# Optimization experiments

Measured on AMD Instinct MI355X. Metric: run time of the kernel, lower is better.

The kernel has to match this reference:

```python
import jax, jax.numpy as jnp
import numpy as np

N, FIN, F, H = 4096, 128, 64, 8
NEG = -1e10


def setup_inputs() -> dict:
    key = jax.random.key(0)
    ks = jax.random.split(key, 6)
    X = jax.random.normal(ks[0], (N, FIN), dtype=jnp.float32)
    # sparse-ish binary adjacency with self loops, stored dense (as the layer expects)
    A = (jax.random.uniform(ks[1], (N, N)) < 0.05).astype(jnp.int32)
    A = A.at[jnp.arange(N), jnp.arange(N)].set(1)
    W = jax.random.normal(ks[2], (H, FIN, F), dtype=jnp.float32) * (1.0 / np.sqrt(FIN))
    b = jnp.zeros((H, F), dtype=jnp.float32)
    a_self = jax.random.normal(ks[3], (H, F), dtype=jnp.float32) * (1.0 / np.sqrt(F))
    a_neigh = jax.random.normal(ks[4], (H, F), dtype=jnp.float32) * (1.0 / np.sqrt(F))
    return {"X": X, "A": A, "W": W, "b": b, "a_self": a_self, "a_neigh": a_neigh}


def reference(X, A, W, b, a_self, a_neigh):
    # Dropout layers run in inference mode in the original call -> identity.
    feats = jnp.einsum('nf,hfo->hno', X, W)              # [H, N, F]
    s_self = jnp.einsum('hno,ho->hn', feats, a_self)     # [H, N]
    s_neigh = jnp.einsum('hno,ho->hn', feats, a_neigh)   # [H, N]
    scores = s_self[:, :, None] + s_neigh[:, None, :]    # [H, N, N]
    scores = jnp.where(scores > 0, scores, 0.2 * scores)  # LeakyReLU(0.2)
    mask = (1.0 - A.astype(jnp.float32)) * NEG            # [N, N]
    attn = jax.nn.softmax(scores + mask[None], axis=-1)   # [H, N, N]
    out = jnp.einsum('hnm,hmo->hno', attn, feats) + b[:, None, :]
    out = jax.nn.elu(out)                                 # [H, N, F]
    # concat heads -> [N, H*F]
    return jnp.transpose(out, (1, 0, 2)).reshape(N, H * F)
```

## Files before the change

kernel.cpp:

```cpp
#include <hip/hip_runtime.h>
#include <cmath>


#define NN 4096
#define FIN 128
#define FF 64
#define HH 8

typedef _Float16 h2 __attribute__((ext_vector_type(2)));
typedef _Float16 h4 __attribute__((ext_vector_type(4)));
typedef _Float16 h8 __attribute__((ext_vector_type(8)));
typedef float f32x4 __attribute__((ext_vector_type(4)));

union H8 {
  h8 v;
  h2 p[4];
};
union H4 {
  h4 v;
  h2 p[2];
};

static __device__ __forceinline__ float dot2acc(h2 a, float c) {
#if __has_builtin(__builtin_amdgcn_fdot2)
  return __builtin_amdgcn_fdot2(a, (h2){(_Float16)1.f, (_Float16)1.f}, c,
                                false);
#else
  return c + (float)a[0] + (float)a[1];
#endif
}

__global__ __launch_bounds__(256) void pack_kernel(
    const int* __restrict__ A, unsigned long long* __restrict__ bits) {
  const int row = blockIdx.x;
  const int wave = threadIdx.x >> 6, lane = threadIdx.x & 63;
  const int* ar = A + (size_t)row * NN;
#pragma unroll
  for (int g = 0; g < 4; ++g) {
    const int w0 = wave * 16 + g * 4;
    int v0 = ar[(w0 + 0) * 64 + lane];
    int v1 = ar[(w0 + 1) * 64 + lane];
    int v2 = ar[(w0 + 2) * 64 + lane];
    int v3 = ar[(w0 + 3) * 64 + lane];
    unsigned long long m0 = __ballot(v0 != 0);
    unsigned long long m1 = __ballot(v1 != 0);
    unsigned long long m2 = __ballot(v2 != 0);
    unsigned long long m3 = __ballot(v3 != 0);
    if (lane == 0) {
      bits[(row << 6) + w0 + 0] = m0;
      bits[(row << 6) + w0 + 1] = m1;
      bits[(row << 6) + w0 + 2] = m2;
      bits[(row << 6) + w0 + 3] = m3;
    }
  }
}

__global__ __launch_bounds__(256) void feats_kernel(
    const float* __restrict__ X, const float* __restrict__ W,
    const float* __restrict__ a_self, const float* __restrict__ a_neigh,
    _Float16* __restrict__ feats_sw, _Float16* __restrict__ es_h,
    _Float16* __restrict__ esn_h, _Float16* __restrict__ et_h,
    _Float16* __restrict__ etn_h) {
  const int h = blockIdx.y, r0 = blockIdx.x * 128;
  const int tid = threadIdx.x, wave = tid >> 6, lane = tid & 63;
  const int l16 = lane & 15, quad = lane >> 4;

  __shared__ _Float16 Xh[128][136];
  __shared__ _Float16 Wt[64][136];

  for (int i = tid; i < 128 * 32; i += 256) {
    int row = i >> 5, c4 = (i & 31) << 2;
    f32x4 x = *(const f32x4*)(X + (size_t)(r0 + row) * FIN + c4);
    h4 hx = {(_Float16)x[0], (_Float16)x[1], (_Float16)x[2], (_Float16)x[3]};
    *(h4*)&Xh[row][c4] = hx;
  }
  for (int i = tid; i < 128 * 16; i += 256) {
    int k = i >> 4, f4 = (i & 15) << 2;
    f32x4 w = *(const f32x4*)(W + (size_t)(h * FIN + k) * FF + f4);
#pragma unroll
    for (int j = 0; j < 4; ++j) Wt[f4 + j][k] = (_Float16)w[j];
  }
  __syncthreads();

  f32x4 acc[2][4];
#pragma unroll
  for (int rg = 0; rg < 2; ++rg)
#pragma unroll
    for (int nb = 0; nb < 4; ++nb) acc[rg][nb] = (f32x4){0.f, 0.f, 0.f, 0.f};

#pragma unroll
  for (int kt = 0; kt < 4; ++kt) {
    const int kof = kt * 32 + quad * 8;
    h8 A0 = *(const h8*)&Xh[wave * 32 + l16][kof];
    h8 A1 = *(const h8*)&Xh[wave * 32 + 16 + l16][kof];
#pragma unroll
    for (int nb = 0; nb < 4; ++nb) {
      h8 B = *(const h8*)&Wt[nb * 16 + l16][kof];
      acc[0][nb] = __builtin_amdgcn_mfma_f32_16x16x32_f16(A0, B, acc[0][nb], 0, 0, 0);
      acc[1][nb] = __builtin_amdgcn_mfma_f32_16x16x32_f16(A1, B, acc[1][nb], 0, 0, 0);
    }
  }

  float as[4], an[4];
#pragma unroll
  for (int nb = 0; nb < 4; ++nb) {
    as[nb] = a_self[h * FF + nb * 16 + l16];
    an[nb] = a_neigh[h * FF + nb * 16 + l16];
  }
#pragma unroll
  for (int rg = 0; rg < 2; ++rg)
#pragma unroll
    for (int r = 0; r < 4; ++r) {
      float ps = acc[rg][0][r] * as[0] + acc[rg][1][r] * as[1] +
                 acc[rg][2][r] * as[2] + acc[rg][3][r] * as[3];
      float pn = acc[rg][0][r] * an[0] + acc[rg][1][r] * an[1] +
                 acc[rg][2][r] * an[2] + acc[rg][3][r] * an[3];
#pragma unroll
      for (int m = 1; m <= 8; m <<= 1) {
        ps += __shfl_xor(ps, m, 64);
        pn += __shfl_xor(pn, m, 64);
      }
      if (l16 == 0) {
        int node = h * NN + r0 + wave * 32 + rg * 16 + quad * 4 + r;
        es_h[node] = (_Float16)__expf(ps - 2.0f);
        esn_h[node] = (_Float16)__expf(0.2f * ps - 2.0f);
        et_h[node] = (_Float16)__expf(pn - 2.0f);
        etn_h[node] = (_Float16)__expf(0.2f * pn - 2.0f);
      }
    }

  const int kb = (r0 >> 5) + wave;
  const int quad2base = quad >> 1;
  const int jbase = (quad & 1) << 2;
#pragma unroll
  for (int rg = 0; rg < 2; ++rg) {
    const int quad2 = rg * 2 + quad2base;
#pragma unroll
    for (int nb = 0; nb < 4; ++nb) {
      h4 v = {(_Float16)acc[rg][nb][0], (_Float16)acc[rg][nb][1],
              (_Float16)acc[rg][nb][2], (_Float16)acc[rg][nb][3]};
      size_t off = ((size_t)((h * 128 + kb) * 4 + nb) << 9) +
                   ((quad2 * 16 + l16) << 3) + jbase;
      *(h4*)(feats_sw + off) = v;
    }
  }
}

__global__ __launch_bounds__(512, 4) void attn_kernel(
    const unsigned long long* __restrict__ Abits,
    const _Float16* __restrict__ feats_sw, const _Float16* __restrict__ es_h,
    const _Float16* __restrict__ esn_h, const _Float16* __restrict__ et_h,
    const _Float16* __restrict__ etn_h, const float* __restrict__ bias,
    float* __restrict__ out) {
  const int bid = blockIdx.x;
  const int h = bid & 7, n0 = (bid >> 3) << 6;
  const int tid = threadIdx.x, wave = tid >> 6, lane = tid & 63;
  const int l16 = lane & 15, quad = lane >> 4;

  __shared__ h4 lut16[16];
  __shared__ float accL[8][32][66];
  __shared__ float denL[8][64];
  if (tid < 16) {
    h4 m;
#pragma unroll
    for (int j = 0; j < 4; ++j) m[j] = (_Float16)((tid >> j) & 1);
    lut16[tid] = m;
  }
  __syncthreads();

  h2 esp[4], esnp[4];
#pragma unroll
  for (int rg = 0; rg < 4; ++rg) {
    _Float16 e = es_h[h * NN + n0 + rg * 16 + l16];
    _Float16 en = esn_h[h * NN + n0 + rg * 16 + l16];
    esp[rg] = (h2){e, e};
    esnp[rg] = (h2){en, en};
  }

  f32x4 acc[4][4];
  float dsum[4] = {0.f, 0.f, 0.f, 0.f};
#pragma unroll
  for (int rg = 0; rg < 4; ++rg)
#pragma unroll
    for (int nb = 0; nb < 4; ++nb) acc[rg][nb] = (f32x4){0.f, 0.f, 0.f, 0.f};

  const uint2* ab = (const uint2*)Abits;
  const int rowbase = n0 + l16;
  const _Float16* etp = et_h + h * NN + (quad << 3);
  const _Float16* etnp = etn_h + h * NN + (quad << 3);
  const _Float16* fb = feats_sw + ((size_t)h << 18) + (lane << 3);

  for (int ct = wave; ct < 64; ct += 8) {
    uint2 bits[4];
#pragma unroll
    for (int rg = 0; rg < 4; ++rg)
      bits[rg] = ab[((rowbase + rg * 16) << 6) + ct];
    const _Float16* fbt = fb + (ct << 12);
#pragma unroll
    for (int kf = 0; kf < 2; ++kf) {
      H8 ET, ETN;
      ET.v = *(const h8*)(etp + (ct << 6) + kf * 32);
      ETN.v = *(const h8*)(etnp + (ct << 6) + kf * 32);
      const _Float16* fk = fbt + (kf << 11);
      h8 B0 = *(const h8*)(fk);
      h8 B1 = *(const h8*)(fk + 512);
      h8 B2 = *(const h8*)(fk + 1024);
      h8 B3 = *(const h8*)(fk + 1536);
#pragma unroll
      for (int rg = 0; rg < 4; ++rg) {
        unsigned word = kf ? bits[rg].y : bits[rg].x;
        unsigned byt = (word >> (quad << 3)) & 0xFFu;
        H4 mlo, mhi;
        mlo.v = lut16[byt & 15u];
        mhi.v = lut16[byt >> 4];
        H8 P;
#pragma unroll
        for (int p = 0; p < 4; ++p) {
          h2 a = esp[rg] * ET.p[p];
          h2 b = esnp[rg] * ETN.p[p];
          h2 r = __builtin_elementwise_max(a, b);
          h2 pm = r * (p < 2 ? mlo.p[p] : mhi.p[p - 2]);
          P.p[p] = pm;
          dsum[rg] = dot2acc(pm, dsum[rg]);
        }
        acc[rg][0] =
            __builtin_amdgcn_mfma_f32_16x16x32_f16(P.v, B0, acc[rg][0], 0, 0, 0);
        acc[rg][1] =
            __builtin_amdgcn_mfma_f32_16x16x32_f16(P.v, B1, acc[rg][1], 0, 0, 0);
        acc[rg][2] =
            __builtin_amdgcn_mfma_f32_16x16x32_f16(P.v, B2, acc[rg][2], 0, 0, 0);
        acc[rg][3] =
            __builtin_amdgcn_mfma_f32_16x16x32_f16(P.v, B3, acc[rg][3], 0, 0, 0);
      }
    }
  }

#pragma unroll
  for (int rg = 0; rg < 4; ++rg) {
    float d = dsum[rg];
    d += __shfl_xor(d, 16, 64);
    d += __shfl_xor(d, 32, 64);
    if (quad == 0) denL[wave][rg * 16 + l16] = d;
  }

  const int erow = tid >> 4, ec0 = (tid & 15) << 2;
#pragma unroll
  for (int ph = 0; ph < 2; ++ph) {
    __syncthreads();
#pragma unroll
    for (int rg2 = 0; rg2 < 2; ++rg2) {
      int rg = ph * 2 + rg2;
#pragma unroll
      for (int nb = 0; nb < 4; ++nb)
#pragma unroll
        for (int r = 0; r < 4; ++r)
          accL[wave][rg2 * 16 + quad * 4 + r][nb * 16 + l16] = acc[rg][nb][r];
    }
    __syncthreads();
    const int grow = ph * 32 + erow;
    float dn = 0.f;
#pragma unroll
    for (int w = 0; w < 8; ++w) dn += denL[w][grow];
    float inv = 1.0f / dn;
    f32x4 v = (f32x4){0.f, 0.f, 0.f, 0.f};
#pragma unroll
    for (int w = 0; w < 8; ++w) {
      f32x4 t = *(const f32x4*)&accL[w][erow][ec0];
      v += t;
    }
    const f32x4 bv = *(const f32x4*)(bias + h * FF + ec0);
#pragma unroll
    for (int i = 0; i < 4; ++i) {
      float x = v[i] * inv + bv[i];
      v[i] = x > 0.f ? x : (__expf(x) - 1.0f);
    }
    float* op = out + (size_t)(n0 + grow) * (HH * FF) + h * FF + ec0;
    *(f32x4*)op = v;
  }
}

extern "C" void kernel_launch(void* const* d_in, const int* in_sizes, int n_in,
                              void* d_out, int out_size, void* d_ws,
                              size_t ws_size, hipStream_t stream) {
  const float* X = (const float*)d_in[0];
  const int* A = (const int*)d_in[1];
  const float* W = (const float*)d_in[2];
  const float* b = (const float*)d_in[3];
  const float* a_self = (const float*)d_in[4];
  const float* a_neigh = (const float*)d_in[5];
  float* out = (float*)d_out;

  char* ws = (char*)d_ws;
  unsigned long long* Abits = (unsigned long long*)ws;
  _Float16* feats_sw = (_Float16*)(ws + (2u << 20));
  _Float16* es_h = (_Float16*)(ws + (6u << 20));
  _Float16* esn_h = (_Float16*)(ws + (6u << 20) + (64u << 10));
  _Float16* et_h = (_Float16*)(ws + (6u << 20) + (128u << 10));
  _Float16* etn_h = (_Float16*)(ws + (6u << 20) + (192u << 10));

  pack_kernel<<<NN, 256, 0, stream>>>(A, Abits);
  feats_kernel<<<dim3(32, 8), 256, 0, stream>>>(X, W, a_self, a_neigh,
                                                feats_sw, es_h, esn_h, et_h,
                                                etn_h);
  attn_kernel<<<512, 512, 0, stream>>>(Abits, feats_sw, es_h, esn_h, et_h,
                                       etn_h, b, out);
}
```

Measured before the change: 152.5 us.

## Pre-transpose W in pack kernel, drop LDS in feats, shrink attn epilogue LDS

```diff
diff --git a/kernel.cpp b/kernel.cpp
--- a/kernel.cpp
+++ b/kernel.cpp
@@ -10,6 +10,7 @@
 typedef _Float16 h2 __attribute__((ext_vector_type(2)));
 typedef _Float16 h4 __attribute__((ext_vector_type(4)));
 typedef _Float16 h8 __attribute__((ext_vector_type(8)));
+typedef float f32x2 __attribute__((ext_vector_type(2)));
 typedef float f32x4 __attribute__((ext_vector_type(4)));
 
 union H8 {
@@ -31,73 +32,74 @@
 }
 
 __global__ __launch_bounds__(256) void pack_kernel(
-    const int* __restrict__ A, unsigned long long* __restrict__ bits) {
-  const int row = blockIdx.x;
-  const int wave = threadIdx.x >> 6, lane = threadIdx.x & 63;
-  const int* ar = A + (size_t)row * NN;
-#pragma unroll
-  for (int g = 0; g < 4; ++g) {
-    const int w0 = wave * 16 + g * 4;
-    int v0 = ar[(w0 + 0) * 64 + lane];
-    int v1 = ar[(w0 + 1) * 64 + lane];
-    int v2 = ar[(w0 + 2) * 64 + lane];
-    int v3 = ar[(w0 + 3) * 64 + lane];
-    unsigned long long m0 = __ballot(v0 != 0);
-    unsigned long long m1 = __ballot(v1 != 0);
-    unsigned long long m2 = __ballot(v2 != 0);
-    unsigned long long m3 = __ballot(v3 != 0);
-    if (lane == 0) {
-      bits[(row << 6) + w0 + 0] = m0;
-      bits[(row << 6) + w0 + 1] = m1;
-      bits[(row << 6) + w0 + 2] = m2;
-      bits[(row << 6) + w0 + 3] = m3;
+    const int* __restrict__ A, const float* __restrict__ W,
+    unsigned long long* __restrict__ bits, _Float16* __restrict__ Wt16) {
+  const int b = blockIdx.x;
+  const int tid = threadIdx.x;
+  if (b < NN) {
+    const int wave = tid >> 6, lane = tid & 63;
+    const int* ar = A + (size_t)b * NN;
+#pragma unroll
+    for (int g = 0; g < 4; ++g) {
+      const int w0 = wave * 16 + g * 4;
+      int v0 = ar[(w0 + 0) * 64 + lane];
+      int v1 = ar[(w0 + 1) * 64 + lane];
+      int v2 = ar[(w0 + 2) * 64 + lane];
+      int v3 = ar[(w0 + 3) * 64 + lane];
+      unsigned long long m0 = __ballot(v0 != 0);
+      unsigned long long m1 = __ballot(v1 != 0);
+      unsigned long long m2 = __ballot(v2 != 0);
+      unsigned long long m3 = __ballot(v3 != 0);
+      if (lane == 0) {
+        bits[(b << 6) + w0 + 0] = m0;
+        bits[(b << 6) + w0 + 1] = m1;
+        bits[(b << 6) + w0 + 2] = m2;
+        bits[(b << 6) + w0 + 3] = m3;
+      }
+    }
+  } else {
+    const int h0 = (b - NN) * 4;
+    for (int h = h0; h < h0 + 4; ++h) {
+      for (int idx = tid; idx < FIN * (FF / 4); idx += 256) {
+        int k = idx >> 4, f4 = (idx & 15) << 2;
+        f32x4 w = *(const f32x4*)(W + ((size_t)(h * FIN + k)) * FF + f4);
+#pragma unroll
+        for (int j = 0; j < 4; ++j)
+          Wt16[((size_t)(h * FF + f4 + j)) * FIN + k] = (_Float16)w[j];
+      }
     }
   }
 }
 
 __global__ __launch_bounds__(256) void feats_kernel(
-    const float* __restrict__ X, const float* __restrict__ W,
+    const float* __restrict__ X, const _Float16* __restrict__ Wt16,
     const float* __restrict__ a_self, const float* __restrict__ a_neigh,
     _Float16* __restrict__ feats_sw, _Float16* __restrict__ es_h,
     _Float16* __restrict__ esn_h, _Float16* __restrict__ et_h,
     _Float16* __restrict__ etn_h) {
-  const int h = blockIdx.y, r0 = blockIdx.x * 128;
+  const int h = blockIdx.y;
   const int tid = threadIdx.x, wave = tid >> 6, lane = tid & 63;
   const int l16 = lane & 15, quad = lane >> 4;
-
-  __shared__ _Float16 Xh[128][136];
-  __shared__ _Float16 Wt[64][136];
-
-  for (int i = tid; i < 128 * 32; i += 256) {
-    int row = i >> 5, c4 = (i & 31) << 2;
-    f32x4 x = *(const f32x4*)(X + (size_t)(r0 + row) * FIN + c4);
-    h4 hx = {(_Float16)x[0], (_Float16)x[1], (_Float16)x[2], (_Float16)x[3]};
-    *(h4*)&Xh[row][c4] = hx;
-  }
-  for (int i = tid; i < 128 * 16; i += 256) {
-    int k = i >> 4, f4 = (i & 15) << 2;
-    f32x4 w = *(const f32x4*)(W + (size_t)(h * FIN + k) * FF + f4);
-#pragma unroll
-    for (int j = 0; j < 4; ++j) Wt[f4 + j][k] = (_Float16)w[j];
-  }
-  __syncthreads();
-
-  f32x4 acc[2][4];
-#pragma unroll
-  for (int rg = 0; rg < 2; ++rg)
-#pragma unroll
-    for (int nb = 0; nb < 4; ++nb) acc[rg][nb] = (f32x4){0.f, 0.f, 0.f, 0.f};
-
+  const int r0 = blockIdx.x * 64 + wave * 16;
+
+  f32x4 acc[4];
+#pragma unroll
+  for (int nb = 0; nb < 4; ++nb) acc[nb] = (f32x4){0.f, 0.f, 0.f, 0.f};
+
+  const float* xr = X + (size_t)(r0 + l16) * FIN;
+  const _Float16* wb = Wt16 + (size_t)h * FF * FIN;
 #pragma unroll
   for (int kt = 0; kt < 4; ++kt) {
     const int kof = kt * 32 + quad * 8;
-    h8 A0 = *(const h8*)&Xh[wave * 32 + l16][kof];
-    h8 A1 = *(const h8*)&Xh[wave * 32 + 16 + l16][kof];
+    f32x4 x0 = *(const f32x4*)(xr + kof);
+    f32x4 x1 = *(const f32x4*)(xr + kof + 4);
+    h8 Af = {(_Float16)x0[0], (_Float16)x0[1], (_Float16)x0[2],
+             (_Float16)x0[3], (_Float16)x1[0], (_Float16)x1[1],
+             (_Float16)x1[2], (_Float16)x1[3]};
 #pragma unroll
     for (int nb = 0; nb < 4; ++nb) {
-      h8 B = *(const h8*)&Wt[nb * 16 + l16][kof];
-      acc[0][nb] = __builtin_amdgcn_mfma_f32_16x16x32_f16(A0, B, acc[0][nb], 0, 0, 0);
-      acc[1][nb] = __builtin_amdgcn_mfma_f32_16x16x32_f16(A1, B, acc[1][nb], 0, 0, 0);
+      h8 Bf = *(const h8*)(wb + (size_t)(nb * 16 + l16) * FIN + kof);
+      acc[nb] = __builtin_amdgcn_mfma_f32_16x16x32_f16(Af, Bf, acc[nb], 0, 0, 0);
     }
   }
 
@@ -108,41 +110,35 @@
     an[nb] = a_neigh[h * FF + nb * 16 + l16];
   }
 #pragma unroll
-  for (int rg = 0; rg < 2; ++rg)
-#pragma unroll
-    for (int r = 0; r < 4; ++r) {
-      float ps = acc[rg][0][r] * as[0] + acc[rg][1][r] * as[1] +
-                 acc[rg][2][r] * as[2] + acc[rg][3][r] * as[3];
-      float pn = acc[rg][0][r] * an[0] + acc[rg][1][r] * an[1] +
-                 acc[rg][2][r] * an[2] + acc[rg][3][r] * an[3];
-#pragma unroll
-      for (int m = 1; m <= 8; m <<= 1) {
-        ps += __shfl_xor(ps, m, 64);
-        pn += __shfl_xor(pn, m, 64);
-      }
-      if (l16 == 0) {
-        int node = h * NN + r0 + wave * 32 + rg * 16 + quad * 4 + r;
-        es_h[node] = (_Float16)__expf(ps - 2.0f);
-        esn_h[node] = (_Float16)__expf(0.2f * ps - 2.0f);
-        et_h[node] = (_Float16)__expf(pn - 2.0f);
-        etn_h[node] = (_Float16)__expf(0.2f * pn - 2.0f);
-      }
-    }
-
-  const int kb = (r0 >> 5) + wave;
-  const int quad2base = quad >> 1;
+  for (int r = 0; r < 4; ++r) {
+    float ps = acc[0][r] * as[0] + acc[1][r] * as[1] + acc[2][r] * as[2] +
+               acc[3][r] * as[3];
+    float pn = acc[0][r] * an[0] + acc[1][r] * an[1] + acc[2][r] * an[2] +
+               acc[3][r] * an[3];
+#pragma unroll
+    for (int m = 1; m <= 8; m <<= 1) {
+      ps += __shfl_xor(ps, m, 64);
+      pn += __shfl_xor(pn, m, 64);
+    }
+    if (l16 == 0) {
+      int node = h * NN + r0 + quad * 4 + r;
+      es_h[node] = (_Float16)__expf(ps - 2.0f);
+      esn_h[node] = (_Float16)__expf(0.2f * ps - 2.0f);
+      et_h[node] = (_Float16)__expf(pn - 2.0f);
+      etn_h[node] = (_Float16)__expf(0.2f * pn - 2.0f);
+    }
+  }
+
+  const int kb = r0 >> 5;
+  const int quadA = ((r0 >> 4) & 1) * 2 + (quad >> 1);
   const int jbase = (quad & 1) << 2;
 #pragma unroll
-  for (int rg = 0; rg < 2; ++rg) {
-    const int quad2 = rg * 2 + quad2base;
-#pragma unroll
-    for (int nb = 0; nb < 4; ++nb) {
-      h4 v = {(_Float16)acc[rg][nb][0], (_Float16)acc[rg][nb][1],
-              (_Float16)acc[rg][nb][2], (_Float16)acc[rg][nb][3]};
-      size_t off = ((size_t)((h * 128 + kb) * 4 + nb) << 9) +
-                   ((quad2 * 16 + l16) << 3) + jbase;
-      *(h4*)(feats_sw + off) = v;
-    }
+  for (int nb = 0; nb < 4; ++nb) {
+    h4 v = {(_Float16)acc[nb][0], (_Float16)acc[nb][1], (_Float16)acc[nb][2],
+            (_Float16)acc[nb][3]};
+    size_t off = ((size_t)((h * 128 + kb) * 4 + nb) << 9) +
+                 ((quadA * 16 + l16) << 3) + jbase;
+    *(h4*)(feats_sw + off) = v;
   }
 }
 
@@ -158,7 +154,7 @@
   const int l16 = lane & 15, quad = lane >> 4;
 
   __shared__ h4 lut16[16];
-  __shared__ float accL[8][32][66];
+  __shared__ float accL[8][16][66];
   __shared__ float denL[8][64];
   if (tid < 16) {
     h4 m;
@@ -178,7 +174,7 @@
   }
 
   f32x4 acc[4][4];
-  float dsum[4] = {0.f, 0.f, 0.f, 0.f};
+  float dsA[4] = {0.f, 0.f, 0.f, 0.f}, dsB[4] = {0.f, 0.f, 0.f, 0.f};
 #pragma unroll
   for (int rg = 0; rg < 4; ++rg)
 #pragma unroll
@@ -221,7 +217,10 @@
           h2 r = __builtin_elementwise_max(a, b);
           h2 pm = r * (p < 2 ? mlo.p[p] : mhi.p[p - 2]);
           P.p[p] = pm;
-          dsum[rg] = dot2acc(pm, dsum[rg]);
+          if (p & 1)
+            dsB[rg] = dot2acc(pm, dsB[rg]);
+          else
+            dsA[rg] = dot2acc(pm, dsA[rg]);
         }
         acc[rg][0] =
             __builtin_amdgcn_mfma_f32_16x16x32_f16(P.v, B0, acc[rg][0], 0, 0, 0);
@@ -237,45 +236,37 @@
 
 #pragma unroll
   for (int rg = 0; rg < 4; ++rg) {
-    float d = dsum[rg];
+    float d = dsA[rg] + dsB[rg];
     d += __shfl_xor(d, 16, 64);
     d += __shfl_xor(d, 32, 64);
     if (quad == 0) denL[wave][rg * 16 + l16] = d;
   }
 
-  const int erow = tid >> 4, ec0 = (tid & 15) << 2;
-#pragma unroll
-  for (int ph = 0; ph < 2; ++ph) {
+  const int erow = tid >> 5, ec0 = (tid & 31) << 1;
+#pragma unroll
+  for (int ph = 0; ph < 4; ++ph) {
     __syncthreads();
 #pragma unroll
-    for (int rg2 = 0; rg2 < 2; ++rg2) {
-      int rg = ph * 2 + rg2;
-#pragma unroll
-      for (int nb = 0; nb < 4; ++nb)
-#pragma unroll
-        for (int r = 0; r < 4; ++r)
-          accL[wave][rg2 * 16 + quad * 4 + r][nb * 16 + l16] = acc[rg][nb][r];
-    }
+    for (int nb = 0; nb < 4; ++nb)
+#pragma unroll
+      for (int r = 0; r < 4; ++r)
+        accL[wave][quad * 4 + r][nb * 16 + l16] = acc[ph][nb][r];
     __syncthreads();
-    const int grow = ph * 32 + erow;
+    const int grow = ph * 16 + erow;
     float dn = 0.f;
 #pragma unroll
     for (int w = 0; w < 8; ++w) dn += denL[w][grow];
     float inv = 1.0f / dn;
-    f32x4 v = (f32x4){0.f, 0.f, 0.f, 0.f};
-#pragma unroll
-    for (int w = 0; w < 8; ++w) {
-      f32x4 t = *(const f32x4*)&accL[w][erow][ec0];
-      v += t;
-    }
-    const f32x4 bv = *(const f32x4*)(bias + h * FF + ec0);
-#pragma unroll
-    for (int i = 0; i < 4; ++i) {
+    f32x2 v = (f32x2){0.f, 0.f};
+#pragma unroll
+    for (int w = 0; w < 8; ++w) v += *(const f32x2*)&accL[w][erow][ec0];
+    const f32x2 bv = *(const f32x2*)(bias + h * FF + ec0);
+#pragma unroll
+    for (int i = 0; i < 2; ++i) {
       float x = v[i] * inv + bv[i];
       v[i] = x > 0.f ? x : (__expf(x) - 1.0f);
     }
-    float* op = out + (size_t)(n0 + grow) * (HH * FF) + h * FF + ec0;
-    *(f32x4*)op = v;
+    *(f32x2*)(out + (size_t)(n0 + grow) * (HH * FF) + h * FF + ec0) = v;
   }
 }
 
@@ -297,9 +288,10 @@
   _Float16* esn_h = (_Float16*)(ws + (6u << 20) + (64u << 10));
   _Float16* et_h = (_Float16*)(ws + (6u << 20) + (128u << 10));
   _Float16* etn_h = (_Float16*)(ws + (6u << 20) + (192u << 10));
-
-  pack_kernel<<<NN, 256, 0, stream>>>(A, Abits);
-  feats_kernel<<<dim3(32, 8), 256, 0, stream>>>(X, W, a_self, a_neigh,
+  _Float16* Wt16 = (_Float16*)(ws + (6u << 20) + (256u << 10));
+
+  pack_kernel<<<NN + 2, 256, 0, stream>>>(A, W, Abits, Wt16);
+  feats_kernel<<<dim3(64, 8), 256, 0, stream>>>(X, Wt16, a_self, a_neigh,
                                                 feats_sw, es_h, esn_h, et_h,
                                                 etn_h);
   attn_kernel<<<512, 512, 0, stream>>>(Abits, feats_sw, es_h, esn_h, et_h,
```

After: 164.1 us. 1.08x slower.
